# Kernel tuning notes

Measured on AMD Instinct MI355X. Metric: run time of the kernel, lower is better.

The kernel has to match this reference:

```python
import jax, jax.numpy as jnp
import numpy as np

E = 200      # embsize
R = 480      # num relations
T = 8        # cur_ts (history length)
N = 40000    # num entities
B = 1024     # batch of triples
NEG_INF = -1.0e9


def _lin(x, W, b):
    # torch nn.Linear convention: y = x @ W.T + b
    return x @ W.T + b


def _gru_cell(x, h, wih, whh, bih, bhh):
    # torch GRUCell: gates packed as [r, z, n]
    gi = x @ wih.T + bih
    gh = h @ whh.T + bhh
    i_r, i_z, i_n = jnp.split(gi, 3, axis=1)
    h_r, h_z, h_n = jnp.split(gh, 3, axis=1)
    r = jax.nn.sigmoid(i_r + h_r)
    z = jax.nn.sigmoid(i_z + h_z)
    n = jnp.tanh(i_n + r * h_n)
    return (1.0 - z) * n + z * h


def setup_inputs() -> dict:
    key = jax.random.key(0)
    ks = jax.random.split(key, 24)
    s = 0.05
    pre_emb = jax.random.normal(ks[0], (N, E), dtype=jnp.float32)
    r_emb = jax.random.normal(ks[1], (R, E), dtype=jnp.float32)
    partial_embeding = jax.random.randint(ks[2], (B, T * R), 0, 2).astype(jnp.float32)
    sub = jax.random.randint(ks[3], (B,), 0, N)
    rel = jax.random.randint(ks[4], (B,), 0, R)
    obj = jax.random.randint(ks[5], (B,), 0, N)
    all_triples = jnp.stack([sub, rel, obj], axis=1).astype(jnp.int64)
    params = {
        'W1': jax.random.normal(ks[6], (2 * E, E)) * s, 'b1': jnp.zeros((2 * E,)),
        'W2': jax.random.normal(ks[7], (E, 2 * E)) * s, 'b2': jnp.zeros((E,)),
        'Wa': jax.random.normal(ks[8], (E, E)) * s, 'ba': jnp.zeros((E,)),
        'Wh1': jax.random.normal(ks[9], (E, E)) * s, 'bh1': jnp.zeros((E,)),
        'Wh2': jax.random.normal(ks[10], (E, E)) * s, 'bh2': jnp.zeros((E,)),
        'Wal': jax.random.normal(ks[11], (E, E)) * s, 'bal': jnp.zeros((E,)),
        'gru_wih': jax.random.normal(ks[12], (3 * E, E)) * s,
        'gru_whh': jax.random.normal(ks[13], (3 * E, E)) * s,
        'gru_bih': jnp.zeros((3 * E,)),
        'gru_bhh': jnp.zeros((3 * E,)),
    }
    params = {k: v.astype(jnp.float32) for k, v in params.items()}
    out = {'pre_emb': pre_emb, 'r_emb': r_emb, 'partial_embeding': partial_embeding,
           'all_triples': all_triples, 'cur_ts': T, 'num_rel': R}
    out.update(params)
    return out


def reference(pre_emb, r_emb, partial_embeding, all_triples, cur_ts, num_rel,
              W1, b1, W2, b2, Wa, ba, Wh1, bh1, Wh2, bh2, Wal, bal,
              gru_wih, gru_whh, gru_bih, gru_bhh):
    mapped_rel = _lin(_lin(r_emb, W1, b1), W2, b2)          # [R, E]
    q_rel = mapped_rel[all_triples[:, 1]]                    # [B, E]
    b = partial_embeding.shape[0]

    # loop-invariant attention base: linear_attn(q_rel) @ mapped_rel^T -> [B, R]
    base = _lin(q_rel, Wa, ba) @ mapped_rel.T

    # [B, cur_ts*R] -> [cur_ts, B, R] for scan over timesteps
    pe = partial_embeding.reshape(b, cur_ts, num_rel).transpose(1, 0, 2)

    def step(h, cur):
        attn = cur * base
        attn = jnp.where(attn == 0, jnp.float32(NEG_INF), attn)
        a = jax.nn.softmax(attn, axis=1)
        x = a @ mapped_rel                                   # [B, E]
        h = _gru_cell(x, h, gru_wih, gru_whh, gru_bih, gru_bhh)
        return h, None

    h0 = jnp.zeros((b, mapped_rel.shape[1]), dtype=pre_emb.dtype)
    gru_hidden, _ = jax.lax.scan(step, h0, pe)

    predicted_hist = 0.1 * _lin(_lin(q_rel, Wh1, bh1), Wh2, bh2) + q_rel
    match_loss = jnp.mean((predicted_hist - gru_hidden) ** 2)

    # forward_forth (distmult scoring)
    gru_hidden2 = _gru_cell(q_rel, predicted_hist, gru_wih, gru_whh, gru_bih, gru_bhh)
    sub_emb = pre_emb[all_triples[:, 0]]
    score_logits = (_lin(sub_emb, Wal, bal) * gru_hidden2) @ _lin(pre_emb, Wal, bal).T  # [B, N]
    score = jax.nn.sigmoid(score_logits)

    labels = jnp.zeros_like(score_logits).at[jnp.arange(b), all_triples[:, 2]].set(1.0)
    # stable BCE(sigmoid(s), y)
    path_loss = -jnp.mean(labels * jax.nn.log_sigmoid(score_logits)
                          + (1.0 - labels) * jax.nn.log_sigmoid(-score_logits))
    return (match_loss, path_loss, score)
```

## Files before the change

kernel.cpp:

```cpp
#include <hip/hip_runtime.h>
#include <hip/hip_bf16.h>
#include <math.h>

#define EE 200
#define RR 480
#define TT 8
#define NN 40000
#define BB 1024
#define KP 224
#define GP 672
#define GPR 704
#define LDS_STRIDE 232

typedef __attribute__((ext_vector_type(8))) short short8v;
typedef __attribute__((ext_vector_type(4))) float f32x4;

__device__ inline unsigned short f2bf(float x) {
    unsigned int u = __float_as_uint(x);
    unsigned int r = ((u >> 16) & 1u) + 0x7fffu;
    return (unsigned short)((u + r) >> 16);
}
__device__ inline float bf2f(unsigned short h) {
    return __uint_as_float(((unsigned int)h) << 16);
}
__device__ inline float sigm(float x) { return 1.0f / (1.0f + __expf(-x)); }
__device__ inline void split_store(unsigned short* hi, unsigned short* lo, size_t i, float v) {
    unsigned short h = f2bf(v);
    hi[i] = h;
    lo[i] = f2bf(v - bf2f(h));
}

struct PrepPtrs {
    unsigned short *W1h, *W1l, *W2h, *W2l, *Wabh, *Wabl, *Wh2h, *Wh2l;
    unsigned short *Walh, *Wall, *WTh, *WTl, *wgh, *wgl, *whg, *whl;
    float *bab, *bihp, *bhhp;
    unsigned short *mapSh, *mapSl, *wgiSh, *wgiSl;
    double* acc;
};

__global__ __launch_bounds__(256) void prep_kernel(
    const float* __restrict__ W1, const float* __restrict__ W2,
    const float* __restrict__ Wa, const float* __restrict__ Wh1,
    const float* __restrict__ Wh2, const float* __restrict__ Wal,
    const float* __restrict__ bal, const float* __restrict__ wih,
    const float* __restrict__ whh, const float* __restrict__ ba,
    const float* __restrict__ bh1, const float* __restrict__ bih,
    const float* __restrict__ bhh, PrepPtrs p)
{
    const int gt = blockIdx.x * 256 + threadIdx.x;
    const int gs = gridDim.x * 256;

    for (int i = gt; i < 448 * 224; i += gs) {
        int r = i / 224, c = i - r * 224;
        split_store(p.W1h, p.W1l, i, (r < 400 && c < 200) ? W1[r * 200 + c] : 0.f);
        float vab = 0.f;
        if (c < 200) {
            if (r < 200) vab = Wa[r * 200 + c];
            else if (r >= 224 && r < 424) vab = Wh1[(r - 224) * 200 + c];
        }
        split_store(p.Wabh, p.Wabl, i, vab);
    }
    for (int i = gt; i < 256 * 416; i += gs) {
        int r = i / 416, c = i - r * 416;
        split_store(p.W2h, p.W2l, i, (r < 200 && c < 400) ? W2[r * 400 + c] : 0.f);
    }
    for (int i = gt; i < 256 * 224; i += gs) {
        int r = i / 224, c = i - r * 224;
        bool in = (r < 200 && c < 200);
        split_store(p.Wh2h, p.Wh2l, i, in ? Wh2[r * 200 + c] : 0.f);
        split_store(p.Walh, p.Wall, i, in ? Wal[r * 200 + c] : 0.f);
        float vt = in ? Wal[c * 200 + r] : ((r == 200 && c < 200) ? bal[c] : 0.f);
        split_store(p.WTh, p.WTl, i, vt);
    }
    for (int i = gt; i < 672 * 224; i += gs) {
        int rr = i / 224, c = i - rr * 224;
        int g = rr / 224, j = rr - g * 224;
        bool in = (j < 200 && c < 200);
        split_store(p.wgh, p.wgl, i, in ? wih[(size_t)(g * 200 + j) * 200 + c] : 0.f);
        split_store(p.whg, p.whl, i, in ? whh[(size_t)(g * 200 + j) * 200 + c] : 0.f);
    }
    for (int i = gt; i < 448; i += gs) {
        float v = 0.f;
        if (i < 200) v = ba[i];
        else if (i >= 224 && i < 424) v = bh1[i - 224];
        p.bab[i] = v;
    }
    for (int i = gt; i < GPR; i += gs) {
        int g = i / 224, j = i - g * 224;
        p.bihp[i] = (g < 3 && j < 200) ? bih[g * 200 + j] : 0.f;
    }
    for (int i = gt; i < GP; i += gs) {
        int g = i / 224, j = i - g * 224;
        p.bhhp[i] = (j < 200) ? bhh[g * 200 + j] : 0.f;
    }
    for (int i = gt; i < 512 * 224; i += gs) { p.mapSh[i] = 0; p.mapSl[i] = 0; }
    for (int i = gt; i < 704 * 480; i += gs) { p.wgiSh[i] = 0; p.wgiSl[i] = 0; }
    if (gt == 0) { p.acc[0] = 0.0; p.acc[1] = 0.0; }
}

template <int MODE, int OUT, int GATHER, int GATEPAD, int EGATHER>
__global__ __launch_bounds__(256) void mfma_flyA(
    const float* __restrict__ A, int lda, const int* __restrict__ gidx, int gsel,
    const unsigned short* __restrict__ Bhi, const unsigned short* __restrict__ Blo,
    const float* __restrict__ bias,
    float* __restrict__ Cf, unsigned short* __restrict__ Chi, unsigned short* __restrict__ Clo,
    int M, int N, int Ka, int Ks,
    const float* __restrict__ extra, int eld, float alpha, int obf)
{
    const int tid = threadIdx.x;
    const int wave = tid >> 6, lane = tid & 63;
    const int r16 = lane & 15, kq = lane >> 4;
    const int kbase = kq * 8;
    const int bm = blockIdx.y * 64 + wave * 16;
    const int bn = blockIdx.x * 64;

    int arow = bm + r16;
    const bool avalid = arow < M;
    if (GATHER) { if (avalid) arow = gidx[arow * 3 + gsel]; }
    const float* Ap = A + (size_t)arow * lda;

    f32x4 acc[4] = {{0,0,0,0},{0,0,0,0},{0,0,0,0},{0,0,0,0}};
    const int nk = Ks >> 5;

    for (int kk = 0; kk < nk; kk++) {
        const int k0 = kk * 32 + kbase;
        short8v a0, a1;
        #pragma unroll
        for (int e = 0; e < 8; e++) {
            float v = (avalid && (k0 + e) < Ka) ? Ap[k0 + e] : 0.f;
            unsigned short h = f2bf(v);
            a0[e] = (short)h;
            a1[e] = (short)f2bf(v - bf2f(h));
        }
        #pragma unroll
        for (int nf = 0; nf < 4; nf++) {
            const size_t boff = (size_t)(bn + nf * 16 + r16) * Ks + k0;
            short8v b0 = *(const short8v*)(Bhi + boff);
            short8v b1 = *(const short8v*)(Blo + boff);
            acc[nf] = __builtin_amdgcn_mfma_f32_16x16x32_bf16(a0, b1, acc[nf], 0, 0, 0);
            acc[nf] = __builtin_amdgcn_mfma_f32_16x16x32_bf16(a1, b0, acc[nf], 0, 0, 0);
            acc[nf] = __builtin_amdgcn_mfma_f32_16x16x32_bf16(a0, b0, acc[nf], 0, 0, 0);
        }
    }

    #pragma unroll
    for (int r = 0; r < 4; r++) {
        const int orow = bm + kq * 4 + r;
        if (orow >= M) continue;
        #pragma unroll
        for (int nf = 0; nf < 4; nf++) {
            const int col = bn + nf * 16 + r16;
            float v = acc[nf][r];
            if (OUT == 0) {
                if (col < N) {
                    if (bias) v += bias[col];
                    if (MODE == 1) {
                        float ex = EGATHER ? extra[(size_t)gidx[orow * 3 + gsel] * eld + col]
                                           : extra[(size_t)orow * eld + col];
                        v = alpha * v + ex;
                    } else if (MODE == 2) {
                        v = v * extra[(size_t)orow * eld + col];
                    }
                    Cf[(size_t)orow * N + col] = v;
                }
            } else if (OUT == 1) {
                if (col < obf) {
                    float w = 0.f;
                    if (col < N) { w = v; if (bias) w += bias[col]; }
                    Chi[(size_t)orow * obf + col] = f2bf(w);
                }
            } else if (OUT == 2) {
                if (col < N) {
                    int wr = GATEPAD ? (orow / 200) * 224 + orow % 200 : orow;
                    if (bias) v += bias[col];
                    split_store(Chi, Clo, (size_t)wr * obf + col, v);
                }
            } else if (OUT == 3) {
                if (col < N) {
                    if (bias) v += bias[col];
                    Cf[(size_t)orow * N + col] = v;
                    split_store(Chi, Clo, (size_t)orow * obf + col, v);
                }
            }
        }
    }
}

__global__ __launch_bounds__(256) void mfma_linear1_kernel(
    const unsigned short* __restrict__ Ahi,
    const unsigned short* __restrict__ Bhi,
    const float* __restrict__ bias, float* __restrict__ C,
    int M, int N, int Ks)
{
    const int tid  = threadIdx.x;
    const int wave = tid >> 6;
    const int lane = tid & 63;
    const int r16   = lane & 15;
    const int khalf = lane >> 4;
    const int kbase = khalf * 8;
    const int bm = blockIdx.y * 64 + wave * 16;
    const int bn = blockIdx.x * 64;

    const unsigned short* ah = Ahi + (size_t)(bm + r16) * Ks + kbase;
    const unsigned short* bh = Bhi + (size_t)(bn + r16) * Ks + kbase;

    f32x4 acc[4] = {{0,0,0,0},{0,0,0,0},{0,0,0,0},{0,0,0,0}};

    for (int k0 = 0; k0 < Ks; k0 += 32) {
        short8v a0 = *(const short8v*)(ah + k0);
        #pragma unroll
        for (int nf = 0; nf < 4; nf++) {
            short8v b0 = *(const short8v*)(bh + (size_t)nf * 16 * Ks + k0);
            acc[nf] = __builtin_amdgcn_mfma_f32_16x16x32_bf16(a0, b0, acc[nf], 0, 0, 0);
        }
    }
    #pragma unroll
    for (int r = 0; r < 4; r++) {
        const int row = bm + khalf * 4 + r;
        #pragma unroll
        for (int nf = 0; nf < 4; nf++) {
            const int col = bn + nf * 16 + r16;
            if (col < N)
                C[(size_t)row * N + col] = acc[nf][r] + (bias ? bias[col] : 0.0f);
        }
    }
}

__global__ __launch_bounds__(832) void scan_all_kernel(
    const unsigned short* __restrict__ Whi, const unsigned short* __restrict__ Wlo,
    const float* __restrict__ bhh_pad,
    const float* __restrict__ gi_all,
    float* __restrict__ h_fin)
{
    __shared__ float hsm[16][228];
    const int tid = threadIdx.x;
    const int wave = tid >> 6;
    const int lane = tid & 63;
    const int r16 = lane & 15, kq = lane >> 4;
    const int brow = blockIdx.x * 16;
    const int jf = wave;
    const int j = jf * 16 + r16;

    for (int i = tid; i < 16 * 228; i += 832) ((float*)hsm)[i] = 0.0f;
    __syncthreads();

    const float br = bhh_pad[j], bz = bhh_pad[224 + j], bn_ = bhh_pad[448 + j];

    for (int t = 0; t < TT; t++) {
        short8v ahi[7], alo[7];
        #pragma unroll
        for (int kk = 0; kk < 7; kk++) {
            float v[8];
            *(float4*)&v[0] = *(const float4*)&hsm[r16][kk * 32 + kq * 8];
            *(float4*)&v[4] = *(const float4*)&hsm[r16][kk * 32 + kq * 8 + 4];
            short8v h8, l8;
            #pragma unroll
            for (int e = 0; e < 8; e++) {
                unsigned short hh = f2bf(v[e]);
                h8[e] = (short)hh;
                l8[e] = (short)f2bf(v[e] - bf2f(hh));
            }
            ahi[kk] = h8; alo[kk] = l8;
        }

        f32x4 ar = {0,0,0,0}, az = {0,0,0,0}, an = {0,0,0,0};
        #pragma unroll
        for (int kk = 0; kk < 7; kk++) {
            const size_t rowr = (size_t)(jf * 16 + r16) * KP + kk * 32 + kq * 8;
            const size_t rowz = rowr + (size_t)224 * KP;
            const size_t rown = rowr + (size_t)448 * KP;
            short8v brh = *(const short8v*)(Whi + rowr);
            short8v brl = *(const short8v*)(Wlo + rowr);
            short8v bzh = *(const short8v*)(Whi + rowz);
            short8v bzl = *(const short8v*)(Wlo + rowz);
            short8v bnh = *(const short8v*)(Whi + rown);
            short8v bnl = *(const short8v*)(Wlo + rown);
            ar = __builtin_amdgcn_mfma_f32_16x16x32_bf16(ahi[kk], brl, ar, 0, 0, 0);
            az = __builtin_amdgcn_mfma_f32_16x16x32_bf16(ahi[kk], bzl, az, 0, 0, 0);
            an = __builtin_amdgcn_mfma_f32_16x16x32_bf16(ahi[kk], bnl, an, 0, 0, 0);
            ar = __builtin_amdgcn_mfma_f32_16x16x32_bf16(alo[kk], brh, ar, 0, 0, 0);
            az = __builtin_amdgcn_mfma_f32_16x16x32_bf16(alo[kk], bzh, az, 0, 0, 0);
            an = __builtin_amdgcn_mfma_f32_16x16x32_bf16(alo[kk], bnh, an, 0, 0, 0);
            ar = __builtin_amdgcn_mfma_f32_16x16x32_bf16(ahi[kk], brh, ar, 0, 0, 0);
            az = __builtin_amdgcn_mfma_f32_16x16x32_bf16(ahi[kk], bzh, az, 0, 0, 0);
            an = __builtin_amdgcn_mfma_f32_16x16x32_bf16(ahi[kk], bnh, an, 0, 0, 0);
        }

        const float* gi_t = gi_all + ((size_t)t * BB + brow) * GP;
        float hnew[4];
        #pragma unroll
        for (int q = 0; q < 4; q++) {
            const int row = kq * 4 + q;
            float gir = gi_t[(size_t)row * GP + j];
            float giz = gi_t[(size_t)row * GP + 224 + j];
            float gin = gi_t[(size_t)row * GP + 448 + j];
            float r_ = sigm(gir + ar[q] + br);
            float z_ = sigm(giz + az[q] + bz);
            float n_ = tanhf(gin + r_ * (an[q] + bn_));
            float hold = hsm[row][j];
            hnew[q] = (1.0f - z_) * n_ + z_ * hold;
        }
        __syncthreads();
        if (j < EE) {
            #pragma unroll
            for (int q = 0; q < 4; q++) hsm[kq * 4 + q][j] = hnew[q];
        }
        __syncthreads();
    }

    for (int i = tid; i < 16 * EE; i += 832) {
        int r = i / EE, c = i - r * EE;
        h_fin[(size_t)(brow + r) * EE + c] = hsm[r][c];
    }
}

__global__ __launch_bounds__(256) void gru2_fused_kernel(
    const unsigned short* __restrict__ Wihi, const unsigned short* __restrict__ Wilo,
    const unsigned short* __restrict__ Whhi, const unsigned short* __restrict__ Whlo,
    const float* __restrict__ bih_pad, const float* __restrict__ bhh_pad,
    const int* __restrict__ triples, const float* __restrict__ map,
    const float* __restrict__ hp, const float* __restrict__ hfin,
    float* __restrict__ ghid2, double* __restrict__ accMatch)
{
    __shared__ float red[256];
    const int tid = threadIdx.x;
    const int wave = tid >> 6, lane = tid & 63;
    const int r16 = lane & 15, kq = lane >> 4;
    const int jf = blockIdx.x;
    const int brow = (blockIdx.y * 4 + wave) * 16;
    const int j = jf * 16 + r16;

    f32x4 ir = {0,0,0,0}, iz = {0,0,0,0}, in_ = {0,0,0,0};
    f32x4 hr = {0,0,0,0}, hz = {0,0,0,0}, hn = {0,0,0,0};

    {
        const int xrow = triples[(brow + r16) * 3 + 1];
        const float* xp = map + (size_t)xrow * EE;
        #pragma unroll
        for (int kk = 0; kk < 7; kk++) {
            short8v a0, a1;
            #pragma unroll
            for (int e = 0; e < 8; e++) {
                int k = kk * 32 + kq * 8 + e;
                float v = (k < EE) ? xp[k] : 0.0f;
                unsigned short hhh = f2bf(v);
                a0[e] = (short)hhh;
                a1[e] = (short)f2bf(v - bf2f(hhh));
            }
            const size_t rowr = (size_t)(jf * 16 + r16) * KP + kk * 32 + kq * 8;
            const size_t rowz = rowr + (size_t)224 * KP;
            const size_t rown = rowr + (size_t)448 * KP;
            short8v brh = *(const short8v*)(Wihi + rowr);
            short8v brl = *(const short8v*)(Wilo + rowr);
            short8v bzh = *(const short8v*)(Wihi + rowz);
            short8v bzl = *(const short8v*)(Wilo + rowz);
            short8v bnh = *(const short8v*)(Wihi + rown);
            short8v bnl = *(const short8v*)(Wilo + rown);
            ir = __builtin_amdgcn_mfma_f32_16x16x32_bf16(a0, brl, ir, 0, 0, 0);
            iz = __builtin_amdgcn_mfma_f32_16x16x32_bf16(a0, bzl, iz, 0, 0, 0);
            in_ = __builtin_amdgcn_mfma_f32_16x16x32_bf16(a0, bnl, in_, 0, 0, 0);
            ir = __builtin_amdgcn_mfma_f32_16x16x32_bf16(a1, brh, ir, 0, 0, 0);
            iz = __builtin_amdgcn_mfma_f32_16x16x32_bf16(a1, bzh, iz, 0, 0, 0);
            in_ = __builtin_amdgcn_mfma_f32_16x16x32_bf16(a1, bnh, in_, 0, 0, 0);
            ir = __builtin_amdgcn_mfma_f32_16x16x32_bf16(a0, brh, ir, 0, 0, 0);
            iz = __builtin_amdgcn_mfma_f32_16x16x32_bf16(a0, bzh, iz, 0, 0, 0);
            in_ = __builtin_amdgcn_mfma_f32_16x16x32_bf16(a0, bnh, in_, 0, 0, 0);
        }
    }
    {
        const float* hpp = hp + (size_t)(brow + r16) * EE;
        #pragma unroll
        for (int kk = 0; kk < 7; kk++) {
            short8v a0, a1;
            #pragma unroll
            for (int e = 0; e < 8; e++) {
                int k = kk * 32 + kq * 8 + e;
                float v = (k < EE) ? hpp[k] : 0.0f;
                unsigned short hhh = f2bf(v);
                a0[e] = (short)hhh;
                a1[e] = (short)f2bf(v - bf2f(hhh));
            }
            const size_t rowr = (size_t)(jf * 16 + r16) * KP + kk * 32 + kq * 8;
            const size_t rowz = rowr + (size_t)224 * KP;
            const size_t rown = rowr + (size_t)448 * KP;
            short8v brh = *(const short8v*)(Whhi + rowr);
            short8v brl = *(const short8v*)(Whlo + rowr);
            short8v bzh = *(const short8v*)(Whhi + rowz);
            short8v bzl = *(const short8v*)(Whlo + rowz);
            short8v bnh = *(const short8v*)(Whhi + rown);
            short8v bnl = *(const short8v*)(Whlo + rown);
            hr = __builtin_amdgcn_mfma_f32_16x16x32_bf16(a0, brl, hr, 0, 0, 0);
            hz = __builtin_amdgcn_mfma_f32_16x16x32_bf16(a0, bzl, hz, 0, 0, 0);
            hn = __builtin_amdgcn_mfma_f32_16x16x32_bf16(a0, bnl, hn, 0, 0, 0);
            hr = __builtin_amdgcn_mfma_f32_16x16x32_bf16(a1, brh, hr, 0, 0, 0);
            hz = __builtin_amdgcn_mfma_f32_16x16x32_bf16(a1, bzh, hz, 0, 0, 0);
            hn = __builtin_amdgcn_mfma_f32_16x16x32_bf16(a1, bnh, hn, 0, 0, 0);
            hr = __builtin_amdgcn_mfma_f32_16x16x32_bf16(a0, brh, hr, 0, 0, 0);
            hz = __builtin_amdgcn_mfma_f32_16x16x32_bf16(a0, bzh, hz, 0, 0, 0);
            hn = __builtin_amdgcn_mfma_f32_16x16x32_bf16(a0, bnh, hn, 0, 0, 0);
        }
    }

    float psum = 0.0f;
    if (j < EE) {
        const float bir = bih_pad[j], biz = bih_pad[224 + j], bin = bih_pad[448 + j];
        const float bhr = bhh_pad[j], bhz = bhh_pad[224 + j], bhn = bhh_pad[448 + j];
        #pragma unroll
        for (int q = 0; q < 4; q++) {
            const int row = brow + kq * 4 + q;
            float r_ = sigm(ir[q] + bir + hr[q] + bhr);
            float z_ = sigm(iz[q] + biz + hz[q] + bhz);
            float n_ = tanhf(in_[q] + bin + r_ * (hn[q] + bhn));
            float hold = hp[(size_t)row * EE + j];
            ghid2[(size_t)row * EE + j] = (1.0f - z_) * n_ + z_ * hold;
            float d = hold - hfin[(size_t)row * EE + j];
            psum += d * d;
        }
    }
    red[tid] = psum;
    __syncthreads();
    for (int s = 128; s > 0; s >>= 1) {
        if (tid < s) red[tid] += red[tid + s];
        __syncthreads();
    }
    if (tid == 0) atomicAdd(accMatch, (double)red[0]);
}

__global__ __launch_bounds__(256) void score_mfma2_kernel(
    const unsigned short* __restrict__ Ubf,
    const float* __restrict__ pre_emb,
    const int* __restrict__ triples,
    float* __restrict__ outScore,
    double* __restrict__ accPath)
{
    __shared__ unsigned short Bs[32 * LDS_STRIDE];
    __shared__ int objs[BB];
    __shared__ float red[256];

    const int tid = threadIdx.x;
    const int bn = blockIdx.x * 32;

    for (int i = tid; i < BB; i += 256) objs[i] = triples[i * 3 + 2];

    for (int idx = tid; idx < 32 * 50; idx += 256) {
        int row = idx / 50;
        int c4 = (idx - row * 50) * 4;
        float4 v = *(const float4*)(pre_emb + (size_t)(bn + row) * EE + c4);
        unsigned short* d = &Bs[row * LDS_STRIDE + c4];
        d[0] = f2bf(v.x); d[1] = f2bf(v.y); d[2] = f2bf(v.z); d[3] = f2bf(v.w);
    }
    for (int idx = tid; idx < 32 * 24; idx += 256) {
        int row = idx / 24;
        int cc = idx - row * 24;
        Bs[row * LDS_STRIDE + 200 + cc] = (cc == 0) ? (unsigned short)0x3F80 : (unsigned short)0;
    }
    __syncthreads();

    const int wave  = tid >> 6;
    const int lane  = tid & 63;
    const int r16   = lane & 15;
    const int khalf = lane >> 4;
    const int kbase = khalf * 8;

    const unsigned short* bs0 = &Bs[( 0 + r16) * LDS_STRIDE + kbase];
    const unsigned short* bs1 = &Bs[(16 + r16) * LDS_STRIDE + kbase];

    float psum = 0.0f;

    for (int mi = 0; mi < 16; mi++) {
        const int m0 = mi * 64 + wave * 16;
        const unsigned short* Ap = Ubf + (size_t)(m0 + r16) * KP + kbase;
        f32x4 acc0 = {0,0,0,0}, acc1 = {0,0,0,0};
        #pragma unroll
        for (int k0 = 0; k0 < KP; k0 += 32) {
            short8v a  = *(const short8v*)(Ap + k0);
            short8v b0 = *(const short8v*)(bs0 + k0);
            short8v b1 = *(const short8v*)(bs1 + k0);
            acc0 = __builtin_amdgcn_mfma_f32_16x16x32_bf16(a, b0, acc0, 0, 0, 0);
            acc1 = __builtin_amdgcn_mfma_f32_16x16x32_bf16(a, b1, acc1, 0, 0, 0);
        }
        #pragma unroll
        for (int r = 0; r < 4; r++) {
            const int grow = m0 + khalf * 4 + r;
            const int objc = objs[grow];
            float xv[2] = { acc0[r], acc1[r] };
            #pragma unroll
            for (int nf = 0; nf < 2; nf++) {
                const int col = bn + nf * 16 + r16;
                float x  = xv[nf];
                float e  = __expf(-fabsf(x));
                float t1 = 1.0f + e;
                float rc = __builtin_amdgcn_rcpf(t1);
                float sig = (x >= 0.0f) ? rc : e * rc;
                float sp = __logf(t1);
                float s  = (col == objc) ? x : -x;
                psum += fminf(s, 0.0f) - sp;
                outScore[(size_t)grow * NN + col] = sig;
            }
        }
    }
    red[tid] = psum;
    __syncthreads();
    for (int s = 128; s > 0; s >>= 1) {
        if (tid < s) red[tid] += red[tid + s];
        __syncthreads();
    }
    if (tid == 0) atomicAdd(accPath, (double)red[0]);
}

__global__ __launch_bounds__(256) void masked_softmax_all_kernel(
    const float* __restrict__ base, const float* __restrict__ part,
    unsigned short* __restrict__ aout_hi)
{
    __shared__ float sv[RR];
    __shared__ float red[256];
    const int blk = blockIdx.x;
    const int b = blk & (BB - 1);
    const int t = blk >> 10;
    const int tid = threadIdx.x;
    const float* brow = base + (size_t)b * RR;
    const float* prow = part + (size_t)b * (TT * RR) + t * RR;

    float lmax = -3.0e38f;
    for (int r = tid; r < RR; r += 256) {
        float v = prow[r] * brow[r];
        if (v == 0.0f) v = -1000000000.0f;
        sv[r] = v;
        lmax = fmaxf(lmax, v);
    }
    red[tid] = lmax;
    __syncthreads();
    for (int s = 128; s > 0; s >>= 1) {
        if (tid < s) red[tid] = fmaxf(red[tid], red[tid + s]);
        __syncthreads();
    }
    float gmax = red[0];
    __syncthreads();

    float lsum = 0.0f;
    for (int r = tid; r < RR; r += 256) {
        float e = __expf(sv[r] - gmax);
        sv[r] = e;
        lsum += e;
    }
    red[tid] = lsum;
    __syncthreads();
    for (int s = 128; s > 0; s >>= 1) {
        if (tid < s) red[tid] += red[tid + s];
        __syncthreads();
    }
    float inv = 1.0f / red[0];
    for (int r = tid; r < RR; r += 256)
        aout_hi[(size_t)blk * RR + r] = f2bf(sv[r] * inv);
}

__global__ void final_kernel(const double* __restrict__ acc, float* __restrict__ out)
{
    if (threadIdx.x == 0) {
        out[0] = (float)(acc[0] / ((double)BB * EE));
        out[1] = (float)(-acc[1] / ((double)BB * NN));
    }
}

extern "C" void kernel_launch(void* const* d_in, const int* in_sizes, int n_in,
                              void* d_out, int out_size, void* d_ws, size_t ws_size,
                              hipStream_t stream) {
    const float* pre_emb = (const float*)d_in[0];
    const float* r_emb   = (const float*)d_in[1];
    const float* part    = (const float*)d_in[2];
    const int*   triples = (const int*)d_in[3];
    const float* W1  = (const float*)d_in[6];
    const float* b1  = (const float*)d_in[7];
    const float* W2  = (const float*)d_in[8];
    const float* b2  = (const float*)d_in[9];
    const float* Wa  = (const float*)d_in[10];
    const float* ba  = (const float*)d_in[11];
    const float* Wh1 = (const float*)d_in[12];
    const float* bh1 = (const float*)d_in[13];
    const float* Wh2 = (const float*)d_in[14];
    const float* bh2 = (const float*)d_in[15];
    const float* Wal = (const float*)d_in[16];
    const float* bal = (const float*)d_in[17];
    const float* wih = (const float*)d_in[18];
    const float* whh = (const float*)d_in[19];
    const float* bih = (const float*)d_in[20];
    const float* bhh = (const float*)d_in[21];

    float* out = (float*)d_out;
    double* acc = (double*)d_ws;
    float* wsf = (float*)d_ws;
    size_t off = 4;
    auto alloc = [&](size_t n) { float* p = wsf + off; off += (n + 3) & ~(size_t)3; return p; };
    auto allocS = [&](size_t n) { return (unsigned short*)alloc((n + 1) / 2); };

    PrepPtrs p;
    p.W1h  = allocS((size_t)448 * 224);
    p.W1l  = allocS((size_t)448 * 224);
    p.W2h  = allocS((size_t)256 * 416);
    p.W2l  = allocS((size_t)256 * 416);
    p.Wabh = allocS((size_t)448 * 224);
    p.Wabl = allocS((size_t)448 * 224);
    p.Wh2h = allocS((size_t)256 * 224);
    p.Wh2l = allocS((size_t)256 * 224);
    p.Walh = allocS((size_t)256 * 224);
    p.Wall = allocS((size_t)256 * 224);
    p.WTh  = allocS((size_t)256 * 224);
    p.WTl  = allocS((size_t)256 * 224);
    p.wgh  = allocS((size_t)GP * KP);
    p.wgl  = allocS((size_t)GP * KP);
    p.whg  = allocS((size_t)GP * KP);
    p.whl  = allocS((size_t)GP * KP);
    p.bab  = alloc(448);
    p.bihp = alloc(GPR);
    p.bhhp = alloc(GP);
    p.mapSh = allocS((size_t)512 * 224);
    p.mapSl = allocS((size_t)512 * 224);
    p.wgiSh = allocS((size_t)GPR * RR);
    p.wgiSl = allocS((size_t)GPR * RR);
    p.acc = acc;

    float* h1     = alloc((size_t)RR * 400);
    float* map    = alloc((size_t)RR * EE);
    float* qa_ph1 = alloc((size_t)BB * 448);
    float* basep  = alloc((size_t)BB * RR);
    unsigned short* aw_hi = allocS((size_t)TT * BB * RR);
    float* gi_all = alloc((size_t)TT * BB * GP);
    float* hfin   = alloc((size_t)BB * EE);
    float* pred   = alloc((size_t)BB * EE);
    float* ghid2  = alloc((size_t)BB * EE);
    float* s1h    = alloc((size_t)BB * EE);
    unsigned short* u_bf = allocS((size_t)BB * KP);

    dim3 blk(256);

    prep_kernel<<<1024, blk, 0, stream>>>(
        W1, W2, Wa, Wh1, Wh2, Wal, bal, wih, whh, ba, bh1, bih, bhh, p);

    mfma_flyA<0,0,0,0,0><<<dim3(7, 8), blk, 0, stream>>>(
        r_emb, 200, nullptr, 0, p.W1h, p.W1l, b1, h1, nullptr, nullptr,
        RR, 400, 200, 224, nullptr, 0, 0.f, 0);
    mfma_flyA<0,3,0,0,0><<<dim3(4, 8), blk, 0, stream>>>(
        h1, 400, nullptr, 0, p.W2h, p.W2l, b2, map, p.mapSh, p.mapSl,
        RR, EE, 400, 416, nullptr, 0, 0.f, 224);
    mfma_flyA<0,0,1,0,0><<<dim3(7, 16), blk, 0, stream>>>(
        map, 200, triples, 1, p.Wabh, p.Wabl, p.bab, qa_ph1, nullptr, nullptr,
        BB, 448, 200, 224, nullptr, 0, 0.f, 0);
    mfma_flyA<0,0,0,0,0><<<dim3(8, 16), blk, 0, stream>>>(
        qa_ph1, 448, nullptr, 0, p.mapSh, p.mapSl, nullptr, basep, nullptr, nullptr,
        BB, RR, 200, 224, nullptr, 0, 0.f, 0);
    masked_softmax_all_kernel<<<TT * BB, blk, 0, stream>>>(basep, part, aw_hi);
    mfma_flyA<0,2,0,1,0><<<dim3(8, 10), blk, 0, stream>>>(
        wih, 200, nullptr, 0, p.mapSh, p.mapSl, nullptr, nullptr, p.wgiSh, p.wgiSl,
        600, RR, 200, 224, nullptr, 0, 0.f, RR);
    mfma_linear1_kernel<<<dim3(11, TT * BB / 64), blk, 0, stream>>>(
        aw_hi, p.wgiSh, p.bihp, gi_all, TT * BB, GP, RR);

    scan_all_kernel<<<BB / 16, dim3(832), 0, stream>>>(
        p.whg, p.whl, p.bhhp, gi_all, hfin);

    mfma_flyA<1,0,0,0,1><<<dim3(4, 16), blk, 0, stream>>>(
        qa_ph1 + 224, 448, triples, 1, p.Wh2h, p.Wh2l, bh2, pred, nullptr, nullptr,
        BB, EE, 200, 224, map, 200, 0.1f, 0);
    gru2_fused_kernel<<<dim3(13, BB / 64), blk, 0, stream>>>(
        p.wgh, p.wgl, p.whg, p.whl, p.bihp, p.bhhp,
        triples, map, pred, hfin, ghid2, acc + 0);
    mfma_flyA<2,0,1,0,0><<<dim3(4, 16), blk, 0, stream>>>(
        pre_emb, 200, triples, 0, p.Walh, p.Wall, bal, s1h, nullptr, nullptr,
        BB, EE, 200, 224, ghid2, 200, 0.f, 0);
    mfma_flyA<0,1,0,0,0><<<dim3(4, 16), blk, 0, stream>>>(
        s1h, 200, nullptr, 0, p.WTh, p.WTl, nullptr, nullptr, u_bf, nullptr,
        BB, KP, 200, 224, nullptr, 0, 0.f, KP);
    score_mfma2_kernel<<<NN / 32, blk, 0, stream>>>(u_bf, pre_emb, triples, out + 2, acc + 1);
    final_kernel<<<1, 64, 0, stream>>>(acc, out);
}
```

Measured before the change: 452.2 us.

## Split GRU scan across grid with cooperative launch and global hidden-state ping-pong

Replaces the per-batch-tile GRU recurrence kernel (64 blocks of 832 threads holding h in LDS) with a cooperative kernel of 13x16 blocks that splits the hidden dimension across blocks. The hidden state is stored as pre-split bf16 hi/lo pairs in global ping-pong buffers and exchanged through a grid-wide sync each timestep. The aim is to spread the recurrence over more CUs and drop the per-step float-to-bf16 split work. In exchange it adds eight grid barriers plus global memory round trips, and it needs extra zero-initialisation in prep.

```diff
diff --git a/kernel.cpp b/kernel.cpp
--- a/kernel.cpp
+++ b/kernel.cpp
@@ -1,5 +1,6 @@
 #include <hip/hip_runtime.h>
 #include <hip/hip_bf16.h>
+#include <hip/hip_cooperative_groups.h>
 #include <math.h>
 
 #define EE 200
@@ -34,7 +35,7 @@
     unsigned short *W1h, *W1l, *W2h, *W2l, *Wabh, *Wabl, *Wh2h, *Wh2l;
     unsigned short *Walh, *Wall, *WTh, *WTl, *wgh, *wgl, *whg, *whl;
     float *bab, *bihp, *bhhp;
-    unsigned short *mapSh, *mapSl, *wgiSh, *wgiSl;
+    unsigned short *mapSh, *mapSl, *wgiSh, *wgiSl, *hbufs;
     double* acc;
 };
 
@@ -95,6 +96,7 @@
     }
     for (int i = gt; i < 512 * 224; i += gs) { p.mapSh[i] = 0; p.mapSl[i] = 0; }
     for (int i = gt; i < 704 * 480; i += gs) { p.wgiSh[i] = 0; p.wgiSl[i] = 0; }
+    for (int i = gt; i < 4 * BB * KP; i += gs) p.hbufs[i] = 0;
     if (gt == 0) { p.acc[0] = 0.0; p.acc[1] = 0.0; }
 }
 
@@ -226,91 +228,89 @@
     }
 }
 
-__global__ __launch_bounds__(832) void scan_all_kernel(
+__global__ __launch_bounds__(256) void scan_coop_kernel(
     const unsigned short* __restrict__ Whi, const unsigned short* __restrict__ Wlo,
     const float* __restrict__ bhh_pad,
     const float* __restrict__ gi_all,
+    unsigned short* ha_hi, unsigned short* ha_lo,
+    unsigned short* hb_hi, unsigned short* hb_lo,
     float* __restrict__ h_fin)
 {
-    __shared__ float hsm[16][228];
+    cooperative_groups::grid_group grid = cooperative_groups::this_grid();
     const int tid = threadIdx.x;
-    const int wave = tid >> 6;
-    const int lane = tid & 63;
+    const int wave = tid >> 6, lane = tid & 63;
     const int r16 = lane & 15, kq = lane >> 4;
-    const int brow = blockIdx.x * 16;
-    const int jf = wave;
+    const int jf = blockIdx.x;
+    const int brow = (blockIdx.y * 4 + wave) * 16;
     const int j = jf * 16 + r16;
 
-    for (int i = tid; i < 16 * 228; i += 832) ((float*)hsm)[i] = 0.0f;
-    __syncthreads();
-
     const float br = bhh_pad[j], bz = bhh_pad[224 + j], bn_ = bhh_pad[448 + j];
 
+    const unsigned short* hin_hi = ha_hi;
+    const unsigned short* hin_lo = ha_lo;
+    unsigned short* hout_hi = hb_hi;
+    unsigned short* hout_lo = hb_lo;
+
     for (int t = 0; t < TT; t++) {
-        short8v ahi[7], alo[7];
-        #pragma unroll
-        for (int kk = 0; kk < 7; kk++) {
-            float v[8];
-            *(float4*)&v[0] = *(const float4*)&hsm[r16][kk * 32 + kq * 8];
-            *(float4*)&v[4] = *(const float4*)&hsm[r16][kk * 32 + kq * 8 + 4];
-            short8v h8, l8;
+        f32x4 ar = {0,0,0,0}, az = {0,0,0,0}, an = {0,0,0,0};
+        if (t > 0) {
+            short8v ahi[7], alo[7];
+            const unsigned short* hh = hin_hi + (size_t)(brow + r16) * KP + kq * 8;
+            const unsigned short* hl = hin_lo + (size_t)(brow + r16) * KP + kq * 8;
             #pragma unroll
-            for (int e = 0; e < 8; e++) {
-                unsigned short hh = f2bf(v[e]);
-                h8[e] = (short)hh;
-                l8[e] = (short)f2bf(v[e] - bf2f(hh));
+            for (int kk = 0; kk < 7; kk++) {
+                ahi[kk] = *(const short8v*)(hh + kk * 32);
+                alo[kk] = *(const short8v*)(hl + kk * 32);
             }
-            ahi[kk] = h8; alo[kk] = l8;
-        }
-
-        f32x4 ar = {0,0,0,0}, az = {0,0,0,0}, an = {0,0,0,0};
-        #pragma unroll
-        for (int kk = 0; kk < 7; kk++) {
-            const size_t rowr = (size_t)(jf * 16 + r16) * KP + kk * 32 + kq * 8;
-            const size_t rowz = rowr + (size_t)224 * KP;
-            const size_t rown = rowr + (size_t)448 * KP;
-            short8v brh = *(const short8v*)(Whi + rowr);
-            short8v brl = *(const short8v*)(Wlo + rowr);
-            short8v bzh = *(const short8v*)(Whi + rowz);
-            short8v bzl = *(const short8v*)(Wlo + rowz);
-            short8v bnh = *(const short8v*)(Whi + rown);
-            short8v bnl = *(const short8v*)(Wlo + rown);
-            ar = __builtin_amdgcn_mfma_f32_16x16x32_bf16(ahi[kk], brl, ar, 0, 0, 0);
-            az = __builtin_amdgcn_mfma_f32_16x16x32_bf16(ahi[kk], bzl, az, 0, 0, 0);
-            an = __builtin_amdgcn_mfma_f32_16x16x32_bf16(ahi[kk], bnl, an, 0, 0, 0);
-            ar = __builtin_amdgcn_mfma_f32_16x16x32_bf16(alo[kk], brh, ar, 0, 0, 0);
-            az = __builtin_amdgcn_mfma_f32_16x16x32_bf16(alo[kk], bzh, az, 0, 0, 0);
-            an = __builtin_amdgcn_mfma_f32_16x16x32_bf16(alo[kk], bnh, an, 0, 0, 0);
-            ar = __builtin_amdgcn_mfma_f32_16x16x32_bf16(ahi[kk], brh, ar, 0, 0, 0);
-            az = __builtin_amdgcn_mfma_f32_16x16x32_bf16(ahi[kk], bzh, az, 0, 0, 0);
-            an = __builtin_amdgcn_mfma_f32_16x16x32_bf16(ahi[kk], bnh, an, 0, 0, 0);
-        }
-
-        const float* gi_t = gi_all + ((size_t)t * BB + brow) * GP;
-        float hnew[4];
+            #pragma unroll
+            for (int kk = 0; kk < 7; kk++) {
+                const size_t rowr = (size_t)(jf * 16 + r16) * KP + kk * 32 + kq * 8;
+                const size_t rowz = rowr + (size_t)224 * KP;
+                const size_t rown = rowr + (size_t)448 * KP;
+                short8v brh = *(const short8v*)(Whi + rowr);
+                short8v brl = *(const short8v*)(Wlo + rowr);
+                short8v bzh = *(const short8v*)(Whi + rowz);
+                short8v bzl = *(const short8v*)(Wlo + rowz);
+                short8v bnh = *(const short8v*)(Whi + rown);
+                short8v bnl = *(const short8v*)(Wlo + rown);
+                ar = __builtin_amdgcn_mfma_f32_16x16x32_bf16(ahi[kk], brl, ar, 0, 0, 0);
+                az = __builtin_amdgcn_mfma_f32_16x16x32_bf16(ahi[kk], bzl, az, 0, 0, 0);
+                an = __builtin_amdgcn_mfma_f32_16x16x32_bf16(ahi[kk], bnl, an, 0, 0, 0);
+                ar = __builtin_amdgcn_mfma_f32_16x16x32_bf16(alo[kk], brh, ar, 0, 0, 0);
+                az = __builtin_amdgcn_mfma_f32_16x16x32_bf16(alo[kk], bzh, az, 0, 0, 0);
+                an = __builtin_amdgcn_mfma_f32_16x16x32_bf16(alo[kk], bnh, an, 0, 0, 0);
+                ar = __builtin_amdgcn_mfma_f32_16x16x32_bf16(ahi[kk], brh, ar, 0, 0, 0);
+                az = __builtin_amdgcn_mfma_f32_16x16x32_bf16(ahi[kk], bzh, az, 0, 0, 0);
+                an = __builtin_amdgcn_mfma_f32_16x16x32_bf16(ahi[kk], bnh, an, 0, 0, 0);
+            }
+        }
+
+        const float* gi_t = gi_all + (size_t)t * BB * GP;
         #pragma unroll
         for (int q = 0; q < 4; q++) {
-            const int row = kq * 4 + q;
+            const int row = brow + kq * 4 + q;
             float gir = gi_t[(size_t)row * GP + j];
             float giz = gi_t[(size_t)row * GP + 224 + j];
             float gin = gi_t[(size_t)row * GP + 448 + j];
             float r_ = sigm(gir + ar[q] + br);
             float z_ = sigm(giz + az[q] + bz);
             float n_ = tanhf(gin + r_ * (an[q] + bn_));
-            float hold = hsm[row][j];
-            hnew[q] = (1.0f - z_) * n_ + z_ * hold;
-        }
-        __syncthreads();
-        if (j < EE) {
-            #pragma unroll
-            for (int q = 0; q < 4; q++) hsm[kq * 4 + q][j] = hnew[q];
-        }
-        __syncthreads();
-    }
-
-    for (int i = tid; i < 16 * EE; i += 832) {
-        int r = i / EE, c = i - r * EE;
-        h_fin[(size_t)(brow + r) * EE + c] = hsm[r][c];
+            float hold = 0.0f;
+            if (t > 0)
+                hold = bf2f(hin_hi[(size_t)row * KP + j]) + bf2f(hin_lo[(size_t)row * KP + j]);
+            float hnew = (1.0f - z_) * n_ + z_ * hold;
+            if (j < EE) {
+                unsigned short nh = f2bf(hnew);
+                hout_hi[(size_t)row * KP + j] = nh;
+                hout_lo[(size_t)row * KP + j] = f2bf(hnew - bf2f(nh));
+                if (t == TT - 1) h_fin[(size_t)row * EE + j] = hnew;
+            }
+        }
+        __threadfence();
+        grid.sync();
+        const unsigned short* th = hin_hi; const unsigned short* tl = hin_lo;
+        hin_hi = hout_hi; hin_lo = hout_lo;
+        hout_hi = (unsigned short*)th; hout_lo = (unsigned short*)tl;
     }
 }
 
@@ -617,7 +617,13 @@
     p.mapSl = allocS((size_t)512 * 224);
     p.wgiSh = allocS((size_t)GPR * RR);
     p.wgiSl = allocS((size_t)GPR * RR);
+    p.hbufs = allocS((size_t)4 * BB * KP);
     p.acc = acc;
+
+    unsigned short* ha_hi = p.hbufs;
+    unsigned short* ha_lo = p.hbufs + (size_t)BB * KP;
+    unsigned short* hb_hi = p.hbufs + (size_t)2 * BB * KP;
+    unsigned short* hb_lo = p.hbufs + (size_t)3 * BB * KP;
 
     float* h1     = alloc((size_t)RR * 400);
     float* map    = alloc((size_t)RR * EE);
@@ -655,8 +661,13 @@
     mfma_linear1_kernel<<<dim3(11, TT * BB / 64), blk, 0, stream>>>(
         aw_hi, p.wgiSh, p.bihp, gi_all, TT * BB, GP, RR);
 
-    scan_all_kernel<<<BB / 16, dim3(832), 0, stream>>>(
-        p.whg, p.whl, p.bhhp, gi_all, hfin);
+    {
+        void* kargs[] = { (void*)&p.whg, (void*)&p.whl, (void*)&p.bhhp, (void*)&gi_all,
+                          (void*)&ha_hi, (void*)&ha_lo, (void*)&hb_hi, (void*)&hb_lo,
+                          (void*)&hfin };
+        hipLaunchCooperativeKernel((void*)scan_coop_kernel, dim3(13, 16), dim3(256),
+                                   kargs, 0, stream);
+    }
 
     mfma_flyA<1,0,0,0,1><<<dim3(4, 16), blk, 0, stream>>>(
         qa_ph1 + 224, 448, triples, 1, p.Wh2h, p.Wh2l, bh2, pred, nullptr, nullptr,
```

New measurement: 798.8 us. +76.7%, slower.
